# Kernel optimization log

Measured on AMD Instinct MI355X. Metric: run time of the kernel, lower is better.

## Reference

```python
import jax, jax.numpy as jnp
import numpy as np

N_NODES = 100000
N_EDGES = 3200000
D_FEAT = 128
N_LAYERS = 2

def setup_inputs() -> dict:
    key = jax.random.key(0)
    k1, k2, k3, k4 = jax.random.split(key, 4)
    x = jax.random.normal(k1, (N_NODES, D_FEAT), dtype=jnp.float32)
    edge_row = jax.random.randint(k2, (N_EDGES,), 0, N_NODES)  # destination (spmm output row)
    edge_col = jax.random.randint(k3, (N_EDGES,), 0, N_NODES)  # source node
    edge_vals = jax.random.uniform(k4, (N_EDGES,), dtype=jnp.float32)
    scalars = jnp.ones((N_LAYERS,), dtype=jnp.float32)  # per-layer learned scalar (init ones)
    return {"x": x, "edge_row": edge_row, "edge_col": edge_col,
            "edge_vals": edge_vals, "scalars": scalars}

def reference(x, edge_row, edge_col, edge_vals, scalars):
    # ScalarSGC forward with dropout p=0 (identity). Same adjacency each layer.
    for l in range(N_LAYERS):
        h = scalars[l] * x                      # scalar * x
        msg = edge_vals[:, None] * h[edge_col]  # [E, D] gather + scale
        agg = jax.ops.segment_sum(msg, edge_row, num_segments=N_NODES)  # spmm
        x = jax.nn.elu(agg)
    return x
```

## Files before the change

### kernel.cpp

```cpp
#include <hip/hip_runtime.h>
#include <math.h>
#include <stdint.h>


#define D_FEAT 128
#define D2     64
#define SCAN_TILE 1024

#define PB 512
#define PT 256
#define RB_BITS 9
#define ROWS_PER_BUCKET 512
#define COL_BITS 17

__device__ __forceinline__ uint32_t f2bf(float f) {
    uint32_t u = __float_as_uint(f);
    return (u + 0x7FFFu + ((u >> 16) & 1u)) >> 16;
}
__device__ __forceinline__ float bf_lo(uint32_t w) { return __uint_as_float(w << 16); }
__device__ __forceinline__ float bf_hi(uint32_t w) { return __uint_as_float(w & 0xFFFF0000u); }

__global__ void convert_kernel(const float2* __restrict__ xin, uint32_t* __restrict__ xbf, int n2) {
    int i = blockIdx.x * blockDim.x + threadIdx.x;
    if (i < n2) {
        float2 f = xin[i];
        xbf[i] = f2bf(f.x) | (f2bf(f.y) << 16);
    }
}

__global__ __launch_bounds__(PT) void coarse_count_kernel(const int* __restrict__ row,
                                                          int* __restrict__ cnt,
                                                          int E, int nbuck) {
    __shared__ int hist[256];
    const int t = threadIdx.x;
    if (t < nbuck) hist[t] = 0;
    __syncthreads();
    const int stride = PB * PT;
    for (int i = blockIdx.x * PT + t; i < E; i += stride)
        atomicAdd(&hist[row[i] >> RB_BITS], 1);
    __syncthreads();
    if (t < nbuck) cnt[t * PB + blockIdx.x] = hist[t];
}

__global__ __launch_bounds__(SCAN_TILE) void scan1_kernel(const int* __restrict__ counts,
                                                          int* __restrict__ excl,
                                                          int* __restrict__ tileSums, int n) {
    __shared__ int wsum[16];
    const int tid  = threadIdx.x;
    const int lane = tid & 63;
    const int wave = tid >> 6;
    const int i    = blockIdx.x * SCAN_TILE + tid;

    int v = (i < n) ? counts[i] : 0;
    int incl = v;
    #pragma unroll
    for (int off = 1; off < 64; off <<= 1) {
        int t = __shfl_up(incl, off, 64);
        if (lane >= off) incl += t;
    }
    if (lane == 63) wsum[wave] = incl;
    __syncthreads();
    if (wave == 0) {
        int s = (lane < 16) ? wsum[lane] : 0;
        #pragma unroll
        for (int off = 1; off < 16; off <<= 1) {
            int t = __shfl_up(s, off, 64);
            if (lane >= off) s += t;
        }
        if (lane < 16) wsum[lane] = s;
    }
    __syncthreads();
    int wbase = (wave == 0) ? 0 : wsum[wave - 1];
    if (i < n) excl[i] = wbase + (incl - v);
    if (tid == 0) tileSums[blockIdx.x] = wsum[15];
}

__global__ __launch_bounds__(1024) void scan2_kernel(const int* __restrict__ tileSums,
                                                     int* __restrict__ tileBase,
                                                     int* __restrict__ total_out, int nb) {
    __shared__ int buf[1024];
    const int tid = threadIdx.x;
    int v = (tid < nb) ? tileSums[tid] : 0;
    buf[tid] = v;
    __syncthreads();
    #pragma unroll
    for (int off = 1; off < 1024; off <<= 1) {
        int t = (tid >= off) ? buf[tid - off] : 0;
        __syncthreads();
        buf[tid] += t;
        __syncthreads();
    }
    if (tid < nb) tileBase[tid] = buf[tid] - v;
    if (tid == nb - 1) *total_out = buf[tid];
}

__global__ void scan3_kernel(int* __restrict__ data, const int* __restrict__ tileBase, int n) {
    int i = blockIdx.x * blockDim.x + threadIdx.x;
    if (i < n) data[i] += tileBase[i >> 10];
}

__global__ __launch_bounds__(PT) void partition_kernel(const int* __restrict__ row,
                                                       const int* __restrict__ col,
                                                       const float* __restrict__ val,
                                                       const int* __restrict__ base,
                                                       int2* __restrict__ pack2,
                                                       int E, int nbuck) {
    __shared__ int cur[256];
    const int t = threadIdx.x;
    if (t < nbuck) cur[t] = base[t * PB + blockIdx.x];
    __syncthreads();
    const int stride = PB * PT;
    for (int i = blockIdx.x * PT + t; i < E; i += stride) {
        int r = row[i];
        int pos = atomicAdd(&cur[r >> RB_BITS], 1);
        pack2[pos] = make_int2(col[i] | ((r & (ROWS_PER_BUCKET - 1)) << COL_BITS),
                               __float_as_int(val[i]));
    }
}

__global__ __launch_bounds__(1024) void fine_sort_kernel(const int* __restrict__ base,
                                                         const int2* __restrict__ pack2,
                                                         int2* __restrict__ pack,
                                                         int* __restrict__ offsets,
                                                         int E, int N, int nbuck) {
    __shared__ int buf[1024];
    __shared__ int cur[ROWS_PER_BUCKET];
    const int b = blockIdx.x;
    const int t = threadIdx.x;
    const int start = base[b * PB];
    const int end   = (b == nbuck - 1) ? E : base[(b + 1) * PB];

    buf[t] = 0;
    __syncthreads();
    for (int i = start + t; i < end; i += 1024)
        atomicAdd(&buf[((unsigned)pack2[i].x) >> COL_BITS], 1);
    __syncthreads();

    int v = buf[t];
    for (int off = 1; off < 1024; off <<= 1) {
        int tv = (t >= off) ? buf[t - off] : 0;
        __syncthreads();
        buf[t] += tv;
        __syncthreads();
    }
    int excl = buf[t] - v;
    if (t < ROWS_PER_BUCKET) {
        int r = (b << RB_BITS) + t;
        if (r < N) offsets[r] = start + excl;
        cur[t] = excl;
    }
    if (b == 0 && t == 0) offsets[N] = E;
    __syncthreads();

    for (int i = start + t; i < end; i += 1024) {
        int2 w = pack2[i];
        int lr = ((unsigned)w.x) >> COL_BITS;
        int p = atomicAdd(&cur[lr], 1);
        pack[start + p] = make_int2(w.x & ((1 << COL_BITS) - 1), w.y);
    }
}

template <int OUT_BF16>
__global__ __launch_bounds__(256) void spmm_elu_kernel(
    const int* __restrict__ offsets, const int2* __restrict__ pack,
    const uint32_t* __restrict__ xin, void* __restrict__ xout,
    const float* __restrict__ scalars, int layer, int N) {
    const int wave = threadIdx.x >> 6;
    const int lane = threadIdx.x & 63;
    const int r    = blockIdx.x * 4 + wave;
    if (r >= N) return;

    int e = offsets[r];
    const int end = offsets[r + 1];

    float a0x = 0.f, a0y = 0.f, a1x = 0.f, a1y = 0.f;
    float a2x = 0.f, a2y = 0.f, a3x = 0.f, a3y = 0.f;

    for (; e + 4 <= end; e += 4) {
        int2 p0 = pack[e], p1 = pack[e + 1], p2 = pack[e + 2], p3 = pack[e + 3];
        uint32_t w0 = xin[(size_t)p0.x * D2 + lane];
        uint32_t w1 = xin[(size_t)p1.x * D2 + lane];
        uint32_t w2 = xin[(size_t)p2.x * D2 + lane];
        uint32_t w3 = xin[(size_t)p3.x * D2 + lane];
        float v0 = __int_as_float(p0.y), v1 = __int_as_float(p1.y);
        float v2 = __int_as_float(p2.y), v3 = __int_as_float(p3.y);
        a0x += v0 * bf_lo(w0); a0y += v0 * bf_hi(w0);
        a1x += v1 * bf_lo(w1); a1y += v1 * bf_hi(w1);
        a2x += v2 * bf_lo(w2); a2y += v2 * bf_hi(w2);
        a3x += v3 * bf_lo(w3); a3y += v3 * bf_hi(w3);
    }
    for (; e < end; ++e) {
        int2 p = pack[e];
        uint32_t w = xin[(size_t)p.x * D2 + lane];
        float v = __int_as_float(p.y);
        a0x += v * bf_lo(w); a0y += v * bf_hi(w);
    }

    float ax = (a0x + a1x) + (a2x + a3x);
    float ay = (a0y + a1y) + (a2y + a3y);
    const float s = scalars[layer];
    ax *= s; ay *= s;
    ax = (ax > 0.f) ? ax : (expf(ax) - 1.f);
    ay = (ay > 0.f) ? ay : (expf(ay) - 1.f);

    if (OUT_BF16) {
        ((uint32_t*)xout)[(size_t)r * D2 + lane] = f2bf(ax) | (f2bf(ay) << 16);
    } else {
        ((float2*)xout)[(size_t)r * D2 + lane] = make_float2(ax, ay);
    }
}

extern "C" void kernel_launch(void* const* d_in, const int* in_sizes, int n_in,
                              void* d_out, int out_size, void* d_ws, size_t ws_size,
                              hipStream_t stream) {
    const float* x         = (const float*)d_in[0];
    const int*   edge_row  = (const int*)d_in[1];
    const int*   edge_col  = (const int*)d_in[2];
    const float* edge_vals = (const float*)d_in[3];
    const float* scalars   = (const float*)d_in[4];

    const int N = in_sizes[0] / D_FEAT;
    const int E = in_sizes[1];
    const int nbuck = (N + ROWS_PER_BUCKET - 1) >> RB_BITS;
    const int M = nbuck * PB;
    const int NB = (M + SCAN_TILE - 1) / SCAN_TILE;

    char*  ws  = (char*)d_ws;
    size_t off = 0;
    auto alloc = [&](size_t bytes) -> void* {
        off = (off + 255) & ~(size_t)255;
        void* p = ws + off;
        off += bytes;
        return p;
    };
    int*      offsets  = (int*)alloc((size_t)(N + 1) * sizeof(int));
    int*      cnt      = (int*)alloc((size_t)(M + 1) * sizeof(int));
    int*      tileSums = (int*)alloc((size_t)NB * sizeof(int));
    int*      tileBase = (int*)alloc((size_t)NB * sizeof(int));
    int2*     pack2    = (int2*)alloc((size_t)E * sizeof(int2));
    int2*     pack     = (int2*)alloc((size_t)E * sizeof(int2));
    uint32_t* xbf      = (uint32_t*)alloc((size_t)N * D2 * sizeof(uint32_t));
    uint32_t* hbf      = (uint32_t*)pack2;
    (void)ws_size;

    convert_kernel<<<(N * D2 + 255) / 256, 256, 0, stream>>>((const float2*)x, xbf, N * D2);
    coarse_count_kernel<<<PB, PT, 0, stream>>>(edge_row, cnt, E, nbuck);
    scan1_kernel<<<NB, SCAN_TILE, 0, stream>>>(cnt, cnt, tileSums, M);
    scan2_kernel<<<1, 1024, 0, stream>>>(tileSums, tileBase, cnt + M, NB);
    scan3_kernel<<<(M + 255) / 256, 256, 0, stream>>>(cnt, tileBase, M);
    partition_kernel<<<PB, PT, 0, stream>>>(edge_row, edge_col, edge_vals, cnt, pack2, E, nbuck);
    fine_sort_kernel<<<nbuck, 1024, 0, stream>>>(cnt, pack2, pack, offsets, E, N, nbuck);

    const int nblk = (N + 3) / 4;
    spmm_elu_kernel<1><<<nblk, 256, 0, stream>>>(offsets, pack, xbf, hbf, scalars, 0, N);
    spmm_elu_kernel<0><<<nblk, 256, 0, stream>>>(offsets, pack, hbf, (void*)d_out, scalars, 1, N);
}
```

Baseline: 463.5 us.

## Cache bucket edges in LDS for fine sort, fold scan3 into consumers

```diff
diff --git a/kernel.cpp b/kernel.cpp
--- a/kernel.cpp
+++ b/kernel.cpp
@@ -7,11 +7,12 @@
 #define D2     64
 #define SCAN_TILE 1024
 
-#define PB 512
-#define PT 256
+#define PB 256
+#define PT 1024
 #define RB_BITS 9
 #define ROWS_PER_BUCKET 512
 #define COL_BITS 17
+#define CACHE_CAP 17152
 
 __device__ __forceinline__ uint32_t f2bf(float f) {
     uint32_t u = __float_as_uint(f);
@@ -33,7 +34,7 @@
                                                           int E, int nbuck) {
     __shared__ int hist[256];
     const int t = threadIdx.x;
-    if (t < nbuck) hist[t] = 0;
+    if (t < 256) hist[t] = 0;
     __syncthreads();
     const int stride = PB * PT;
     for (int i = blockIdx.x * PT + t; i < E; i += stride)
@@ -94,20 +95,19 @@
     if (tid == nb - 1) *total_out = buf[tid];
 }
 
-__global__ void scan3_kernel(int* __restrict__ data, const int* __restrict__ tileBase, int n) {
-    int i = blockIdx.x * blockDim.x + threadIdx.x;
-    if (i < n) data[i] += tileBase[i >> 10];
-}
-
 __global__ __launch_bounds__(PT) void partition_kernel(const int* __restrict__ row,
                                                        const int* __restrict__ col,
                                                        const float* __restrict__ val,
-                                                       const int* __restrict__ base,
+                                                       const int* __restrict__ cnt,
+                                                       const int* __restrict__ tileBase,
                                                        int2* __restrict__ pack2,
                                                        int E, int nbuck) {
     __shared__ int cur[256];
     const int t = threadIdx.x;
-    if (t < nbuck) cur[t] = base[t * PB + blockIdx.x];
+    if (t < nbuck) {
+        int idx = t * PB + blockIdx.x;
+        cur[t] = cnt[idx] + tileBase[idx >> 10];
+    }
     __syncthreads();
     const int stride = PB * PT;
     for (int i = blockIdx.x * PT + t; i < E; i += stride) {
@@ -118,22 +118,30 @@
     }
 }
 
-__global__ __launch_bounds__(1024) void fine_sort_kernel(const int* __restrict__ base,
+__global__ __launch_bounds__(1024) void fine_sort_kernel(const int* __restrict__ cnt,
+                                                         const int* __restrict__ tileBase,
                                                          const int2* __restrict__ pack2,
                                                          int2* __restrict__ pack,
                                                          int* __restrict__ offsets,
                                                          int E, int N, int nbuck) {
+    extern __shared__ int2 ecache[];
     __shared__ int buf[1024];
     __shared__ int cur[ROWS_PER_BUCKET];
     const int b = blockIdx.x;
     const int t = threadIdx.x;
-    const int start = base[b * PB];
-    const int end   = (b == nbuck - 1) ? E : base[(b + 1) * PB];
-
+    const int start = cnt[b << 8] + tileBase[b >> 2];
+    const int end   = (b == nbuck - 1) ? E : (cnt[(b + 1) << 8] + tileBase[(b + 1) >> 2]);
+    const int n  = end - start;
+    const int nc = (n < CACHE_CAP) ? n : CACHE_CAP;
+
+    for (int i = t; i < nc; i += 1024) ecache[i] = pack2[start + i];
     buf[t] = 0;
     __syncthreads();
-    for (int i = start + t; i < end; i += 1024)
-        atomicAdd(&buf[((unsigned)pack2[i].x) >> COL_BITS], 1);
+
+    for (int i = t; i < n; i += 1024) {
+        int key = (i < nc) ? ecache[i].x : pack2[start + i].x;
+        atomicAdd(&buf[((unsigned)key) >> COL_BITS], 1);
+    }
     __syncthreads();
 
     int v = buf[t];
@@ -152,8 +160,8 @@
     if (b == 0 && t == 0) offsets[N] = E;
     __syncthreads();
 
-    for (int i = start + t; i < end; i += 1024) {
-        int2 w = pack2[i];
+    for (int i = t; i < n; i += 1024) {
+        int2 w = (i < nc) ? ecache[i] : pack2[start + i];
         int lr = ((unsigned)w.x) >> COL_BITS;
         int p = atomicAdd(&cur[lr], 1);
         pack[start + p] = make_int2(w.x & ((1 << COL_BITS) - 1), w.y);
@@ -166,7 +174,7 @@
     const uint32_t* __restrict__ xin, void* __restrict__ xout,
     const float* __restrict__ scalars, int layer, int N) {
     const int wave = threadIdx.x >> 6;
-    const int lane = threadIdx.x & 63;
+    const uint32_t lane = threadIdx.x & 63;
     const int r    = blockIdx.x * 4 + wave;
     if (r >= N) return;
 
@@ -178,10 +186,10 @@
 
     for (; e + 4 <= end; e += 4) {
         int2 p0 = pack[e], p1 = pack[e + 1], p2 = pack[e + 2], p3 = pack[e + 3];
-        uint32_t w0 = xin[(size_t)p0.x * D2 + lane];
-        uint32_t w1 = xin[(size_t)p1.x * D2 + lane];
-        uint32_t w2 = xin[(size_t)p2.x * D2 + lane];
-        uint32_t w3 = xin[(size_t)p3.x * D2 + lane];
+        uint32_t w0 = xin[(((uint32_t)p0.x) << 6) + lane];
+        uint32_t w1 = xin[(((uint32_t)p1.x) << 6) + lane];
+        uint32_t w2 = xin[(((uint32_t)p2.x) << 6) + lane];
+        uint32_t w3 = xin[(((uint32_t)p3.x) << 6) + lane];
         float v0 = __int_as_float(p0.y), v1 = __int_as_float(p1.y);
         float v2 = __int_as_float(p2.y), v3 = __int_as_float(p3.y);
         a0x += v0 * bf_lo(w0); a0y += v0 * bf_hi(w0);
@@ -191,7 +199,7 @@
     }
     for (; e < end; ++e) {
         int2 p = pack[e];
-        uint32_t w = xin[(size_t)p.x * D2 + lane];
+        uint32_t w = xin[(((uint32_t)p.x) << 6) + lane];
         float v = __int_as_float(p.y);
         a0x += v * bf_lo(w); a0y += v * bf_hi(w);
     }
@@ -247,9 +255,10 @@
     coarse_count_kernel<<<PB, PT, 0, stream>>>(edge_row, cnt, E, nbuck);
     scan1_kernel<<<NB, SCAN_TILE, 0, stream>>>(cnt, cnt, tileSums, M);
     scan2_kernel<<<1, 1024, 0, stream>>>(tileSums, tileBase, cnt + M, NB);
-    scan3_kernel<<<(M + 255) / 256, 256, 0, stream>>>(cnt, tileBase, M);
-    partition_kernel<<<PB, PT, 0, stream>>>(edge_row, edge_col, edge_vals, cnt, pack2, E, nbuck);
-    fine_sort_kernel<<<nbuck, 1024, 0, stream>>>(cnt, pack2, pack, offsets, E, N, nbuck);
+    partition_kernel<<<PB, PT, 0, stream>>>(edge_row, edge_col, edge_vals, cnt, tileBase,
+                                            pack2, E, nbuck);
+    fine_sort_kernel<<<nbuck, 1024, (size_t)CACHE_CAP * sizeof(int2), stream>>>(
+        cnt, tileBase, pack2, pack, offsets, E, N, nbuck);
 
     const int nblk = (N + 3) / 4;
     spmm_elu_kernel<1><<<nblk, 256, 0, stream>>>(offsets, pack, xbf, hbf, scalars, 0, N);
```

New measurement: 436.6 us. 1.06x faster.
